# Optimization experiments

Measured on AMD Instinct MI355X. Metric: run time of the kernel, lower is better.

## Reference

```python
import jax, jax.numpy as jnp
import numpy as np

T, N, F0, H0, H1 = 8, 50000, 128, 128, 64
NNZ, E = 800000, 1000000


def setup_inputs() -> dict:
    key = jax.random.key(0)
    ks = jax.random.split(key, 24)
    s = 0.05  # param scale so sigmoid/tanh gates are not fully saturated
    inp = {
        "X": jax.random.normal(ks[0], (T, N, F0), jnp.float32),
        "A_rows": jax.random.randint(ks[1], (T, NNZ), 0, N, jnp.int32),
        "A_cols": jax.random.randint(ks[2], (T, NNZ), 0, N, jnp.int32),
        "A_val": jax.random.uniform(ks[3], (T, NNZ), jnp.float32),
        "edge_time": jax.random.randint(ks[4], (E,), 0, T, jnp.int32),
        "edge_src": jax.random.randint(ks[5], (E,), 0, N, jnp.int32),
        "edge_trg": jax.random.randint(ks[6], (E,), 0, N, jnp.int32),
        "p": jax.random.normal(ks[7], (F0,), jnp.float32),
        "W_Z": s * jax.random.normal(ks[8], (F0, F0), jnp.float32),
        "U_Z": s * jax.random.normal(ks[9], (F0, F0), jnp.float32),
        "B_Z": s * jax.random.normal(ks[10], (F0, H0), jnp.float32),
        "W_R": s * jax.random.normal(ks[11], (F0, F0), jnp.float32),
        "U_R": s * jax.random.normal(ks[12], (F0, F0), jnp.float32),
        "B_R": s * jax.random.normal(ks[13], (F0, H0), jnp.float32),
        "W_H": s * jax.random.normal(ks[14], (F0, F0), jnp.float32),
        "U_H": s * jax.random.normal(ks[15], (F0, F0), jnp.float32),
        "B_H": s * jax.random.normal(ks[16], (F0, H0), jnp.float32),
        "W_init": s * jax.random.normal(ks[17], (F0, H0), jnp.float32),
        "U": s * jax.random.normal(ks[18], (2 * H0, H1), jnp.float32),
    }
    return inp


def reference(X, A_rows, A_cols, A_val, edge_time, edge_src, edge_trg,
              p, W_Z, U_Z, B_Z, W_R, U_R, B_R, W_H, U_H, B_H, W_init, U):
    Tn, Nn, _ = X.shape
    k = W_init.shape[1]  # topk size == columns of evolving weight
    p_hat = p / jnp.linalg.norm(p)

    def step(W, inputs):
        Xs, rows, cols, vals = inputs  # Xs: [N,F0]; rows/cols/vals: [NNZ]
        # summarize: top-k node rows weighted by projection score
        y = Xs @ p_hat                       # [N]
        topv, idx = jax.lax.top_k(y, k)
        Z = (Xs[idx] * topv[:, None]).T      # [F0,k]
        # GRU-style weight evolution on the [F0,k] weight matrix
        Zg = jax.nn.sigmoid(W_Z @ Z + U_Z @ W + B_Z)
        R = jax.nn.sigmoid(W_R @ Z + U_R @ W + B_R)
        Ht = jnp.tanh(W_H @ Z + U_H @ (R * W) + B_H)
        W_new = (1.0 - Zg) * W + Zg * Ht
        # sparse GCN conv: (A @ Xs) @ W_new  via gather + segment_sum
        AH = jax.ops.segment_sum(vals[:, None] * Xs[cols], rows,
                                 num_segments=Nn)  # [N,F0]
        return W_new, AH @ W_new                   # Y_t: [N,H0]

    W_fin, Y = jax.lax.scan(step, W_init, (X, A_rows, A_cols, A_val))
    Yf = Y.reshape(Tn * Nn, -1)                    # [T*N,H0]
    flat_src = edge_time * Nn + edge_src
    flat_trg = edge_time * Nn + edge_trg
    Y_mat = jnp.concatenate([Yf[flat_src], Yf[flat_trg]], axis=1)  # [E,2*H0]
    output = Y_mat @ U                              # [E,H1]
    return output, W_fin
```

## Files before the change

### kernel.cpp

```cpp
#include <hip/hip_runtime.h>
#include <math.h>

#define T_ 8
#define N_ 50000
#define F0_ 128
#define H0_ 128
#define H1_ 64
#define NNZ_ 800000
#define E_ 1000000
#define K_ 128
#define CAP_ 3072
#define NB 391
#define BCH 8192

__device__ inline unsigned ford(float f) {
    unsigned b = __float_as_uint(f);
    return (b & 0x80000000u) ? ~b : (b | 0x80000000u);
}
__device__ inline float funord(unsigned u) {
    unsigned b = (u & 0x80000000u) ? (u & 0x7fffffffu) : ~u;
    return __uint_as_float(b);
}
__device__ inline unsigned bfr(float f) {
    unsigned u = __float_as_uint(f);
    return (u + 0x7fffu + ((u >> 16) & 1u)) >> 16;
}
__device__ inline unsigned bfpack(float lo, float hi) { return bfr(lo) | (bfr(hi) << 16); }
__device__ inline float bflo(unsigned u) { return __uint_as_float(u << 16); }
__device__ inline float bfhi(unsigned u) { return __uint_as_float(u & 0xffff0000u); }

__global__ void k_phat(const float* p, float* p_hat) {
    __shared__ float s[128];
    int i = threadIdx.x;
    float v = p[i];
    s[i] = v * v;
    __syncthreads();
    for (int off = 64; off > 0; off >>= 1) {
        if (i < off) s[i] += s[i + off];
        __syncthreads();
    }
    p_hat[i] = v / sqrtf(s[0]);
}

__global__ void k_y(const float* __restrict__ X, const float* __restrict__ p_hat,
                    float* __restrict__ y, unsigned* __restrict__ Xh) {
    int gid = blockIdx.x * 256 + threadIdx.x;
    int wave = gid >> 6, lane = gid & 63;
    if (wave >= T_ * N_) return;
    const float2* xr = (const float2*)(X + (size_t)wave * F0_);
    float2 a = xr[lane];
    if (Xh) Xh[(size_t)wave * 64 + lane] = bfpack(a.x, a.y);
    float2 ph = ((const float2*)p_hat)[lane];
    float acc = a.x * ph.x + a.y * ph.y;
#pragma unroll
    for (int off = 32; off > 0; off >>= 1) acc += __shfl_down(acc, off);
    if (lane == 0) y[wave] = acc;
}

__global__ __launch_bounds__(1024) void k_topk(const float* __restrict__ y,
                                               float* __restrict__ topv,
                                               int* __restrict__ topidx) {
    int t = blockIdx.x;
    const float* yt = y + (size_t)t * N_;
    __shared__ int hist[256];
    __shared__ int sb1, sAbove, sP, scand;
    __shared__ unsigned cu[CAP_];
    __shared__ int cidx[CAP_];
    int tid = threadIdx.x;

    if (tid < 256) hist[tid] = 0;
    __syncthreads();
    for (int i = tid; i < N_; i += 1024) {
        unsigned u = ford(yt[i]);
        atomicAdd(&hist[u >> 24], 1);
    }
    __syncthreads();
    if (tid == 0) {
        int acc = 0, b = 255;
        for (; b >= 0; b--) { acc += hist[b]; if (acc >= K_) break; }
        sb1 = b;
        sAbove = acc - hist[b];
    }
    __syncthreads();
    int b1 = sb1;
    if (tid < 256) hist[tid] = 0;
    __syncthreads();
    for (int i = tid; i < N_; i += 1024) {
        unsigned u = ford(yt[i]);
        if ((int)(u >> 24) == b1) atomicAdd(&hist[(u >> 16) & 255], 1);
    }
    __syncthreads();
    if (tid == 0) {
        int acc = sAbove, b = 255;
        for (; b >= 0; b--) { acc += hist[b]; if (acc >= K_) break; }
        sP = (b1 << 8) | b;
        scand = 0;
    }
    __syncthreads();
    unsigned P = (unsigned)sP;
    for (int i = tid; i < N_; i += 1024) {
        unsigned u = ford(yt[i]);
        if ((u >> 16) >= P) {
            int pos = atomicAdd(&scand, 1);
            if (pos < CAP_) { cu[pos] = u; cidx[pos] = i; }
        }
    }
    __syncthreads();
    int C = min(scand, CAP_);
    for (int c = tid; c < C; c += 1024) {
        unsigned uc = cu[c];
        int ic = cidx[c];
        int rank = 0;
        for (int o = 0; o < C; o++) {
            unsigned uo = cu[o];
            rank += (uo > uc) || (uo == uc && cidx[o] < ic);
        }
        if (rank < K_) {
            topv[t * K_ + rank] = funord(uc);
            topidx[t * K_ + rank] = ic;
        }
    }
}

__global__ void k_z(const float* __restrict__ X, const float* __restrict__ topv,
                    const int* __restrict__ topidx, float* __restrict__ Z) {
    int gid = blockIdx.x * 256 + threadIdx.x;
    if (gid >= T_ * F0_ * K_) return;
    int j = gid & 127;
    int f = (gid >> 7) & 127;
    int t = gid >> 14;
    int idx = topidx[t * K_ + j];
    float v = topv[t * K_ + j];
    Z[gid] = X[((size_t)(t * N_ + idx)) * F0_ + f] * v;
}

__global__ void k_az(const float* __restrict__ WZ, const float* __restrict__ WR,
                     const float* __restrict__ WH, const float* __restrict__ BZ,
                     const float* __restrict__ BR, const float* __restrict__ BH,
                     const float* __restrict__ Z, float* __restrict__ AZ,
                     float* __restrict__ AR, float* __restrict__ AHo) {
    int gid = blockIdx.x * 256 + threadIdx.x;
    int j = gid & 127;
    int i = (gid >> 7) & 127;
    int t = (gid >> 14) & 7;
    int g = gid >> 17;
    const float* W = (g == 0) ? WZ : (g == 1) ? WR : WH;
    const float* B = (g == 0) ? BZ : (g == 1) ? BR : BH;
    float* Ao = (g == 0) ? AZ : (g == 1) ? AR : AHo;
    const float* Zt = Z + (size_t)t * 16384;
    float acc = B[i * 128 + j];
    for (int k = 0; k < 128; k++) acc += W[i * 128 + k] * Zt[k * 128 + j];
    Ao[(size_t)(t * 128 + i) * 128 + j] = acc;
}

__global__ __launch_bounds__(512) void k_cnt(const int* __restrict__ A_rows,
                                             int* __restrict__ bcnt) {
    __shared__ int cnt[NB];
    int t = blockIdx.y, ci = blockIdx.x;
    int tid = threadIdx.x;
    for (int i = tid; i < NB; i += 512) cnt[i] = 0;
    __syncthreads();
    int e0 = ci * BCH;
#pragma unroll
    for (int k = 0; k < 16; k++) {
        int idx = e0 + tid + k * 512;
        if (idx < NNZ_) atomicAdd(&cnt[A_rows[(size_t)t * NNZ_ + idx] >> 7], 1);
    }
    __syncthreads();
    for (int b = tid; b < NB; b += 512)
        if (cnt[b]) atomicAdd(&bcnt[t * NB + b], cnt[b]);
}

__global__ __launch_bounds__(512) void k_bscan(const int* __restrict__ bcnt,
                                               int* __restrict__ bbase) {
    int t = blockIdx.x;
    int tid = threadIdx.x;
    __shared__ int buf[512];
    int v = (tid < NB) ? bcnt[t * NB + tid] : 0;
    buf[tid] = v;
    __syncthreads();
    for (int off = 1; off < 512; off <<= 1) {
        int x = (tid >= off) ? buf[tid - off] : 0;
        __syncthreads();
        buf[tid] += x;
        __syncthreads();
    }
    if (tid < NB) bbase[t * NB + tid] = buf[tid] - v;
}

__global__ __launch_bounds__(512) void k_binA(const int* __restrict__ A_rows,
                                              const int* __restrict__ A_cols,
                                              const float* __restrict__ A_val,
                                              const int* __restrict__ bbase,
                                              int* __restrict__ bfill,
                                              int2* __restrict__ ebuck) {
    __shared__ int cnt[NB];
    __shared__ int gbase[NB];
    __shared__ int rbase[NB];
    int t = blockIdx.y, ci = blockIdx.x;
    int tid = threadIdx.x;
    for (int i = tid; i < NB; i += 512) cnt[i] = 0;
    __syncthreads();
    unsigned meta[16];
    float val[16];
    int lrank[16];
    int e0 = ci * BCH;
#pragma unroll
    for (int k = 0; k < 16; k++) {
        int idx = e0 + tid + k * 512;
        meta[k] = 0xFFFFFFFFu;
        val[k] = 0.f;
        lrank[k] = 0;
        if (idx < NNZ_) {
            int r = A_rows[(size_t)t * NNZ_ + idx];
            int c = A_cols[(size_t)t * NNZ_ + idx];
            val[k] = A_val[(size_t)t * NNZ_ + idx];
            int b = r >> 7, rlo = r & 127;
            meta[k] = (unsigned)c | ((unsigned)rlo << 16) | ((unsigned)b << 23);
            lrank[k] = atomicAdd(&cnt[b], 1);
        }
    }
    __syncthreads();
    for (int b = tid; b < NB; b += 512) {
        int n = cnt[b];
        gbase[b] = n ? atomicAdd(&bfill[t * NB + b], n) : 0;
        rbase[b] = bbase[t * NB + b];
    }
    __syncthreads();
#pragma unroll
    for (int k = 0; k < 16; k++) {
        if (meta[k] != 0xFFFFFFFFu) {
            int b = meta[k] >> 23;
            ebuck[(size_t)t * NNZ_ + rbase[b] + gbase[b] + lrank[k]] =
                make_int2((int)meta[k], __float_as_int(val[k]));
        }
    }
}

__global__ __launch_bounds__(256) void k_bsort(const int* __restrict__ bbase,
                                               const int* __restrict__ bcnt,
                                               const int2* __restrict__ ebuck,
                                               int2* __restrict__ ecv,
                                               int* __restrict__ row_ptr) {
    __shared__ int rcnt[128];
    __shared__ int rex[128];
    __shared__ int rfill[128];
    __shared__ int sbuf[128];
    int t = blockIdx.y, b = blockIdx.x;
    int tid = threadIdx.x;
    int r0 = b << 7;
    int nrows = min(128, N_ - r0);
    int base = bbase[t * NB + b];
    int n = bcnt[t * NB + b];
    if (tid < 128) {
        rcnt[tid] = 0;
        rfill[tid] = 0;
    }
    __syncthreads();
    const int2* src = ebuck + (size_t)t * NNZ_ + base;
    int2* dst = ecv + (size_t)t * NNZ_ + base;
    for (int i = tid; i < n; i += 256) atomicAdd(&rcnt[(src[i].x >> 16) & 127], 1);
    __syncthreads();
    if (tid < 128) sbuf[tid] = rcnt[tid];
    __syncthreads();
    for (int off = 1; off < 128; off <<= 1) {
        int x = (tid >= off && tid < 128) ? sbuf[tid - off] : 0;
        __syncthreads();
        if (tid < 128) sbuf[tid] += x;
        __syncthreads();
    }
    if (tid < 128) rex[tid] = sbuf[tid] - rcnt[tid];
    if (tid < nrows) row_ptr[(size_t)t * (N_ + 1) + r0 + tid] = base + sbuf[tid] - rcnt[tid];
    if (b == 0 && tid == 0) row_ptr[(size_t)t * (N_ + 1) + N_] = NNZ_;
    __syncthreads();
    for (int i = tid; i < n; i += 256) {
        int2 e = src[i];
        int rlo = (e.x >> 16) & 127;
        int col = e.x & 0xFFFF;
        int pos = rex[rlo] + atomicAdd(&rfill[rlo], 1);
        dst[pos] = make_int2(col, e.y);
    }
}

__global__ void k_spmm(const unsigned* __restrict__ Xh, const int* __restrict__ row_ptr,
                       const int2* __restrict__ ecv, float* __restrict__ AH) {
    int gid = blockIdx.x * 256 + threadIdx.x;
    int wave = gid >> 6, lane = gid & 63;
    if (wave >= T_ * N_) return;
    int t = wave / N_;
    int r = wave - t * N_;
    int s = row_ptr[(size_t)t * (N_ + 1) + r];
    int len = row_ptr[(size_t)t * (N_ + 1) + r + 1] - s;
    const unsigned* Xt = Xh + (size_t)t * N_ * 64 + lane;
    const int2* ev = ecv + (size_t)t * NNZ_;
    float2 acc = {0.f, 0.f};
    for (int base = 0; base < len; base += 64) {
        int nn = min(64, len - base);
        int2 my = {0, 0};
        if (base + lane < len) my = ev[s + base + lane];
        int q = 0;
        for (; q + 8 <= nn; q += 8) {
            int c0 = __shfl(my.x, q + 0); float v0 = __int_as_float(__shfl(my.y, q + 0));
            int c1 = __shfl(my.x, q + 1); float v1 = __int_as_float(__shfl(my.y, q + 1));
            int c2 = __shfl(my.x, q + 2); float v2 = __int_as_float(__shfl(my.y, q + 2));
            int c3 = __shfl(my.x, q + 3); float v3 = __int_as_float(__shfl(my.y, q + 3));
            int c4 = __shfl(my.x, q + 4); float v4 = __int_as_float(__shfl(my.y, q + 4));
            int c5 = __shfl(my.x, q + 5); float v5 = __int_as_float(__shfl(my.y, q + 5));
            int c6 = __shfl(my.x, q + 6); float v6 = __int_as_float(__shfl(my.y, q + 6));
            int c7 = __shfl(my.x, q + 7); float v7 = __int_as_float(__shfl(my.y, q + 7));
            unsigned x0 = Xt[(size_t)c0 * 64];
            unsigned x1 = Xt[(size_t)c1 * 64];
            unsigned x2 = Xt[(size_t)c2 * 64];
            unsigned x3 = Xt[(size_t)c3 * 64];
            unsigned x4 = Xt[(size_t)c4 * 64];
            unsigned x5 = Xt[(size_t)c5 * 64];
            unsigned x6 = Xt[(size_t)c6 * 64];
            unsigned x7 = Xt[(size_t)c7 * 64];
            acc.x += v0 * bflo(x0); acc.y += v0 * bfhi(x0);
            acc.x += v1 * bflo(x1); acc.y += v1 * bfhi(x1);
            acc.x += v2 * bflo(x2); acc.y += v2 * bfhi(x2);
            acc.x += v3 * bflo(x3); acc.y += v3 * bfhi(x3);
            acc.x += v4 * bflo(x4); acc.y += v4 * bfhi(x4);
            acc.x += v5 * bflo(x5); acc.y += v5 * bfhi(x5);
            acc.x += v6 * bflo(x6); acc.y += v6 * bfhi(x6);
            acc.x += v7 * bflo(x7); acc.y += v7 * bfhi(x7);
        }
        for (; q < nn; q++) {
            int c = __shfl(my.x, q);
            float v = __int_as_float(__shfl(my.y, q));
            unsigned xp = Xt[(size_t)c * 64];
            acc.x += v * bflo(xp);
            acc.y += v * bfhi(xp);
        }
    }
    ((float2*)AH)[(size_t)wave * 64 + lane] = acc;
}

__global__ void k_spmm_f32(const float* __restrict__ X, const int* __restrict__ row_ptr,
                           const int2* __restrict__ ecv, float* __restrict__ AH) {
    int gid = blockIdx.x * 256 + threadIdx.x;
    int wave = gid >> 6, lane = gid & 63;
    if (wave >= T_ * N_) return;
    int t = wave / N_;
    int r = wave - t * N_;
    int s = row_ptr[(size_t)t * (N_ + 1) + r];
    int len = row_ptr[(size_t)t * (N_ + 1) + r + 1] - s;
    const float2* Xt = (const float2*)(X + (size_t)t * N_ * F0_);
    const int2* ev = ecv + (size_t)t * NNZ_;
    float2 acc = {0.f, 0.f};
    for (int base = 0; base < len; base += 64) {
        int nn = min(64, len - base);
        int2 my = {0, 0};
        if (base + lane < len) my = ev[s + base + lane];
        for (int q = 0; q < nn; q++) {
            int c = __shfl(my.x, q);
            float v = __int_as_float(__shfl(my.y, q));
            float2 x = Xt[(size_t)c * 64 + lane];
            acc.x += v * x.x;
            acc.y += v * x.y;
        }
    }
    ((float2*)AH)[(size_t)wave * 64 + lane] = acc;
}

__global__ __launch_bounds__(256) void k_gru(const float* __restrict__ AZt,
                                             const float* __restrict__ ARt,
                                             const float* __restrict__ AHt,
                                             const float* __restrict__ UZ,
                                             const float* __restrict__ UR,
                                             const float* __restrict__ UH,
                                             const float* __restrict__ Wprev,
                                             float* __restrict__ Wnew) {
    __shared__ float RWs[128][2];
    int jl = threadIdx.x >> 7;
    int i = threadIdx.x & 127;
    int j = blockIdx.x * 2 + jl;
    int gid = i * 128 + j;
    float az = AZt[gid], ar = ARt[gid];
    for (int k = 0; k < 128; k++) {
        float w = Wprev[k * 128 + j];
        az += UZ[i * 128 + k] * w;
        ar += UR[i * 128 + k] * w;
    }
    float zg = 1.f / (1.f + expf(-az));
    float rg = 1.f / (1.f + expf(-ar));
    RWs[i][jl] = rg * Wprev[gid];
    __syncthreads();
    float acc = AHt[gid];
    for (int k = 0; k < 128; k++) acc += UH[i * 128 + k] * RWs[k][jl];
    float ht = tanhf(acc);
    float w0 = Wprev[gid];
    Wnew[gid] = (1.f - zg) * w0 + zg * ht;
}

__global__ void k_wu(const float* __restrict__ W_seq, const float* __restrict__ U,
                     float* __restrict__ WU) {
    int blk = blockIdx.x;
    int t = blk >> 7, k = blk & 127;
    int h2 = threadIdx.x;
    const float* Wt = W_seq + (size_t)t * 16384;
    int h = h2 & 63;
    const float* Ub = U + (h2 < 64 ? 0 : 128 * 64);
    float acc = 0.f;
    for (int m = 0; m < 128; m++) acc += Wt[k * 128 + m] * Ub[m * 64 + h];
    WU[((size_t)t * 128 + k) * 128 + h2] = acc;
}

__global__ __launch_bounds__(256) void k_pq(const float* __restrict__ AH,
                                            const float* __restrict__ WU,
                                            unsigned* __restrict__ PQh) {
    __shared__ float AT[32][36];
    __shared__ float WUc[32][128];
    int t = blockIdx.y;
    int rbase = blockIdx.x * 32;
    int tid = threadIdx.x;
    const float* wu = WU + (size_t)t * 16384;
    const float* AHt = AH + (size_t)t * N_ * F0_;
    unsigned* PQt = PQh + (size_t)t * N_ * 64;
    int cg = tid & 31;
    int rg = tid >> 5;
    float4 acc0 = {0.f, 0.f, 0.f, 0.f};
    float4 acc1 = {0.f, 0.f, 0.f, 0.f};
    float4 acc2 = {0.f, 0.f, 0.f, 0.f};
    float4 acc3 = {0.f, 0.f, 0.f, 0.f};
    int srow = tid >> 3;
    int sk4 = (tid & 7) * 4;
    for (int kc = 0; kc < 128; kc += 32) {
        {
            float4 v = {0.f, 0.f, 0.f, 0.f};
            int r = rbase + srow;
            if (r < N_) v = *(const float4*)(AHt + (size_t)r * F0_ + kc + sk4);
            AT[sk4 + 0][srow] = v.x;
            AT[sk4 + 1][srow] = v.y;
            AT[sk4 + 2][srow] = v.z;
            AT[sk4 + 3][srow] = v.w;
        }
        {
            const float4* src = (const float4*)(wu + (size_t)kc * 128);
            float4* dst = (float4*)&WUc[0][0];
            dst[tid] = src[tid];
            dst[tid + 256] = src[tid + 256];
            dst[tid + 512] = src[tid + 512];
            dst[tid + 768] = src[tid + 768];
        }
        __syncthreads();
#pragma unroll 4
        for (int kk = 0; kk < 32; kk++) {
            float4 a = *(const float4*)&AT[kk][rg * 4];
            float4 w = *(const float4*)&WUc[kk][cg * 4];
            acc0.x += a.x * w.x; acc0.y += a.x * w.y; acc0.z += a.x * w.z; acc0.w += a.x * w.w;
            acc1.x += a.y * w.x; acc1.y += a.y * w.y; acc1.z += a.y * w.z; acc1.w += a.y * w.w;
            acc2.x += a.z * w.x; acc2.y += a.z * w.y; acc2.z += a.z * w.z; acc2.w += a.z * w.w;
            acc3.x += a.w * w.x; acc3.y += a.w * w.y; acc3.z += a.w * w.z; acc3.w += a.w * w.w;
        }
        __syncthreads();
    }
    int r0 = rbase + rg * 4;
    if (r0 + 0 < N_) {
        uint2 o = {bfpack(acc0.x, acc0.y), bfpack(acc0.z, acc0.w)};
        *(uint2*)(PQt + (size_t)(r0 + 0) * 64 + cg * 2) = o;
    }
    if (r0 + 1 < N_) {
        uint2 o = {bfpack(acc1.x, acc1.y), bfpack(acc1.z, acc1.w)};
        *(uint2*)(PQt + (size_t)(r0 + 1) * 64 + cg * 2) = o;
    }
    if (r0 + 2 < N_) {
        uint2 o = {bfpack(acc2.x, acc2.y), bfpack(acc2.z, acc2.w)};
        *(uint2*)(PQt + (size_t)(r0 + 2) * 64 + cg * 2) = o;
    }
    if (r0 + 3 < N_) {
        uint2 o = {bfpack(acc3.x, acc3.y), bfpack(acc3.z, acc3.w)};
        *(uint2*)(PQt + (size_t)(r0 + 3) * 64 + cg * 2) = o;
    }
}

__global__ __launch_bounds__(256) void k_pq_f32(float* __restrict__ AH,
                                                const float* __restrict__ WU) {
    __shared__ float AT[32][36];
    __shared__ float WUc[32][128];
    int t = blockIdx.y;
    int rbase = blockIdx.x * 32;
    int tid = threadIdx.x;
    const float* wu = WU + (size_t)t * 16384;
    float* AHt = AH + (size_t)t * N_ * F0_;
    int cg = tid & 31;
    int rg = tid >> 5;
    float4 acc0 = {0.f, 0.f, 0.f, 0.f};
    float4 acc1 = {0.f, 0.f, 0.f, 0.f};
    float4 acc2 = {0.f, 0.f, 0.f, 0.f};
    float4 acc3 = {0.f, 0.f, 0.f, 0.f};
    int srow = tid >> 3;
    int sk4 = (tid & 7) * 4;
    for (int kc = 0; kc < 128; kc += 32) {
        {
            float4 v = {0.f, 0.f, 0.f, 0.f};
            int r = rbase + srow;
            if (r < N_) v = *(const float4*)(AHt + (size_t)r * F0_ + kc + sk4);
            AT[sk4 + 0][srow] = v.x;
            AT[sk4 + 1][srow] = v.y;
            AT[sk4 + 2][srow] = v.z;
            AT[sk4 + 3][srow] = v.w;
        }
        {
            const float4* src = (const float4*)(wu + (size_t)kc * 128);
            float4* dst = (float4*)&WUc[0][0];
            dst[tid] = src[tid];
            dst[tid + 256] = src[tid + 256];
            dst[tid + 512] = src[tid + 512];
            dst[tid + 768] = src[tid + 768];
        }
        __syncthreads();
#pragma unroll 4
        for (int kk = 0; kk < 32; kk++) {
            float4 a = *(const float4*)&AT[kk][rg * 4];
            float4 w = *(const float4*)&WUc[kk][cg * 4];
            acc0.x += a.x * w.x; acc0.y += a.x * w.y; acc0.z += a.x * w.z; acc0.w += a.x * w.w;
            acc1.x += a.y * w.x; acc1.y += a.y * w.y; acc1.z += a.y * w.z; acc1.w += a.y * w.w;
            acc2.x += a.z * w.x; acc2.y += a.z * w.y; acc2.z += a.z * w.z; acc2.w += a.z * w.w;
            acc3.x += a.w * w.x; acc3.y += a.w * w.y; acc3.z += a.w * w.z; acc3.w += a.w * w.w;
        }
        __syncthreads();
    }
    int r0 = rbase + rg * 4;
    if (r0 + 0 < N_) *(float4*)(AHt + (size_t)(r0 + 0) * F0_ + cg * 4) = acc0;
    if (r0 + 1 < N_) *(float4*)(AHt + (size_t)(r0 + 1) * F0_ + cg * 4) = acc1;
    if (r0 + 2 < N_) *(float4*)(AHt + (size_t)(r0 + 2) * F0_ + cg * 4) = acc2;
    if (r0 + 3 < N_) *(float4*)(AHt + (size_t)(r0 + 3) * F0_ + cg * 4) = acc3;
}

__global__ void k_final(const unsigned* __restrict__ PQh, const int* __restrict__ et,
                        const int* __restrict__ es, const int* __restrict__ eg,
                        float* __restrict__ out) {
    int gid = blockIdx.x * 256 + threadIdx.x;
    if (gid >= E_ * 16) return;
    int e = gid >> 4, q = gid & 15;
    int t = et[e];
    const uint2 a = *(const uint2*)(PQh + ((size_t)(t * N_ + es[e])) * 64 + q * 2);
    const uint2 b = *(const uint2*)(PQh + ((size_t)(t * N_ + eg[e])) * 64 + 32 + q * 2);
    float4 o;
    o.x = bflo(a.x) + bflo(b.x);
    o.y = bfhi(a.x) + bfhi(b.x);
    o.z = bflo(a.y) + bflo(b.y);
    o.w = bfhi(a.y) + bfhi(b.y);
    *(float4*)(out + (size_t)e * 64 + q * 4) = o;
}

__global__ void k_final_f32(const float* __restrict__ PQ, const int* __restrict__ et,
                            const int* __restrict__ es, const int* __restrict__ eg,
                            float* __restrict__ out) {
    int gid = blockIdx.x * 256 + threadIdx.x;
    if (gid >= E_ * 16) return;
    int e = gid >> 4, q = gid & 15;
    int t = et[e];
    const float4 a = *(const float4*)(PQ + ((size_t)(t * N_ + es[e])) * 128 + q * 4);
    const float4 b = *(const float4*)(PQ + ((size_t)(t * N_ + eg[e])) * 128 + 64 + q * 4);
    float4 o = {a.x + b.x, a.y + b.y, a.z + b.z, a.w + b.w};
    *(float4*)(out + (size_t)e * 64 + q * 4) = o;
}

__global__ void k_wfin(const float* __restrict__ W_seq, float* __restrict__ out) {
    int gid = blockIdx.x * 256 + threadIdx.x;
    out[(size_t)E_ * 64 + gid] = W_seq[(size_t)7 * 16384 + gid];
}

extern "C" void kernel_launch(void* const* d_in, const int* in_sizes, int n_in,
                              void* d_out, int out_size, void* d_ws, size_t ws_size,
                              hipStream_t stream) {
    const float* X = (const float*)d_in[0];
    const int* A_rows = (const int*)d_in[1];
    const int* A_cols = (const int*)d_in[2];
    const float* A_val = (const float*)d_in[3];
    const int* edge_time = (const int*)d_in[4];
    const int* edge_src = (const int*)d_in[5];
    const int* edge_trg = (const int*)d_in[6];
    const float* p = (const float*)d_in[7];
    const float* W_Z = (const float*)d_in[8];
    const float* U_Z = (const float*)d_in[9];
    const float* B_Z = (const float*)d_in[10];
    const float* W_R = (const float*)d_in[11];
    const float* U_R = (const float*)d_in[12];
    const float* B_R = (const float*)d_in[13];
    const float* W_H = (const float*)d_in[14];
    const float* U_H = (const float*)d_in[15];
    const float* B_H = (const float*)d_in[16];
    const float* W_init = (const float*)d_in[17];
    const float* U = (const float*)d_in[18];
    float* out = (float*)d_out;

    char* ws = (char*)d_ws;
    size_t off = 0;
    auto take = [&](size_t bytes) {
        char* ptr = ws + off;
        off = (off + bytes + 255) & ~(size_t)255;
        return (void*)ptr;
    };
    float* AH = (float*)take((size_t)T_ * N_ * F0_ * 4);
    int2* ecv = (int2*)take((size_t)T_ * NNZ_ * 8);
    float* yv = (float*)take((size_t)T_ * N_ * 4);
    int* row_ptr = (int*)take((size_t)T_ * (N_ + 1) * 4);
    int* bcnt = (int*)take((size_t)T_ * NB * 4);
    int* bbase = (int*)take((size_t)T_ * NB * 4);
    int* bfill = (int*)take((size_t)T_ * NB * 4);
    float* p_hat = (float*)take(512);
    float* topv = (float*)take((size_t)T_ * K_ * 4);
    int* topidx = (int*)take((size_t)T_ * K_ * 4);
    float* Z = (float*)take((size_t)T_ * F0_ * K_ * 4);
    float* AZb = (float*)take((size_t)T_ * 16384 * 4);
    float* ARb = (float*)take((size_t)T_ * 16384 * 4);
    float* AHb = (float*)take((size_t)T_ * 16384 * 4);
    float* W_seq = (float*)take((size_t)T_ * 16384 * 4);
    float* WU = (float*)take((size_t)T_ * 16384 * 4);
    unsigned* Xh = (unsigned*)take((size_t)T_ * N_ * 64 * 4);
    bool use_bf16 = (off <= ws_size);
    unsigned* PQh = Xh;
    int2* ebuck = (int2*)AH;

    hipMemsetAsync(bcnt, 0, (size_t)T_ * NB * 4, stream);
    hipMemsetAsync(bfill, 0, (size_t)T_ * NB * 4, stream);

    k_phat<<<1, 128, 0, stream>>>(p, p_hat);
    k_y<<<(T_ * N_ * 64) / 256, 256, 0, stream>>>(X, p_hat, yv, use_bf16 ? Xh : nullptr);
    k_topk<<<T_, 1024, 0, stream>>>(yv, topv, topidx);
    k_z<<<(T_ * F0_ * K_) / 256, 256, 0, stream>>>(X, topv, topidx, Z);
    k_az<<<(3 * T_ * 16384) / 256, 256, 0, stream>>>(W_Z, W_R, W_H, B_Z, B_R, B_H, Z,
                                                     AZb, ARb, AHb);
    {
        dim3 gA((NNZ_ + BCH - 1) / BCH, T_);
        k_cnt<<<gA, 512, 0, stream>>>(A_rows, bcnt);
        k_bscan<<<T_, 512, 0, stream>>>(bcnt, bbase);
        k_binA<<<gA, 512, 0, stream>>>(A_rows, A_cols, A_val, bbase, bfill, ebuck);
        dim3 gB(NB, T_);
        k_bsort<<<gB, 256, 0, stream>>>(bbase, bcnt, ebuck, ecv, row_ptr);
    }
    if (use_bf16)
        k_spmm<<<(T_ * N_ * 64) / 256, 256, 0, stream>>>(Xh, row_ptr, ecv, AH);
    else
        k_spmm_f32<<<(T_ * N_ * 64) / 256, 256, 0, stream>>>(X, row_ptr, ecv, AH);
    for (int t = 0; t < T_; t++) {
        const float* Wprev = (t == 0) ? W_init : (W_seq + (size_t)(t - 1) * 16384);
        k_gru<<<64, 256, 0, stream>>>(AZb + (size_t)t * 16384, ARb + (size_t)t * 16384,
                                      AHb + (size_t)t * 16384, U_Z, U_R, U_H, Wprev,
                                      W_seq + (size_t)t * 16384);
    }
    k_wu<<<T_ * 128, 128, 0, stream>>>(W_seq, U, WU);
    {
        dim3 g((N_ + 31) / 32, T_);
        if (use_bf16) {
            k_pq<<<g, 256, 0, stream>>>(AH, WU, PQh);
            k_final<<<(E_ * 16) / 256, 256, 0, stream>>>(PQh, edge_time, edge_src,
                                                         edge_trg, out);
        } else {
            k_pq_f32<<<g, 256, 0, stream>>>(AH, WU);
            k_final_f32<<<(E_ * 16) / 256, 256, 0, stream>>>(AH, edge_time, edge_src,
                                                             edge_trg, out);
        }
    }
    k_wfin<<<(F0_ * H0_) / 256, 256, 0, stream>>>(W_seq, out);
}
```

Baseline: 966.5 us.

## Reassociate GCN as A·(X·WU) so SpMM gathers bf16 projected features

Rather than computing AH = A·X in fp32 and then multiplying by WU, the code first computes X·WU densely from the bf16 X copy and stores it as bf16, then runs the sparse gather-accumulate over those rows and writes PQ in bf16. The aim is to halve the SpMM output write (bf16 instead of fp32 AH) and to drop the fp32 AH read in the dense GEMM, since that GEMM now reads bf16 X. It also adds a 16-wide unrolled gather loop. The intermediate X·WU is rounded to bf16 before aggregation, which adds rounding error, and the workspace layout is reorganised so XWU and PQh share the old AH region.

```diff
diff --git a/kernel.cpp b/kernel.cpp
--- a/kernel.cpp
+++ b/kernel.cpp
@@ -282,8 +282,76 @@
     }
 }
 
-__global__ void k_spmm(const unsigned* __restrict__ Xh, const int* __restrict__ row_ptr,
-                       const int2* __restrict__ ecv, float* __restrict__ AH) {
+__global__ __launch_bounds__(256) void k_xwu(const unsigned* __restrict__ Xh,
+                                             const float* __restrict__ WU,
+                                             unsigned* __restrict__ XWU) {
+    __shared__ float AT[32][36];
+    __shared__ float WUc[32][128];
+    int t = blockIdx.y;
+    int rbase = blockIdx.x * 32;
+    int tid = threadIdx.x;
+    const float* wu = WU + (size_t)t * 16384;
+    const unsigned* Xt = Xh + (size_t)t * N_ * 64;
+    unsigned* XWUt = XWU + (size_t)t * N_ * 64;
+    int cg = tid & 31;
+    int rg = tid >> 5;
+    float4 acc0 = {0.f, 0.f, 0.f, 0.f};
+    float4 acc1 = {0.f, 0.f, 0.f, 0.f};
+    float4 acc2 = {0.f, 0.f, 0.f, 0.f};
+    float4 acc3 = {0.f, 0.f, 0.f, 0.f};
+    int srow = tid >> 3;
+    int sk4 = (tid & 7) * 4;
+    for (int kc = 0; kc < 128; kc += 32) {
+        {
+            uint2 u = {0u, 0u};
+            int r = rbase + srow;
+            if (r < N_) u = *(const uint2*)(Xt + (size_t)r * 64 + (kc >> 1) + (sk4 >> 1));
+            AT[sk4 + 0][srow] = bflo(u.x);
+            AT[sk4 + 1][srow] = bfhi(u.x);
+            AT[sk4 + 2][srow] = bflo(u.y);
+            AT[sk4 + 3][srow] = bfhi(u.y);
+        }
+        {
+            const float4* src = (const float4*)(wu + (size_t)kc * 128);
+            float4* dst = (float4*)&WUc[0][0];
+            dst[tid] = src[tid];
+            dst[tid + 256] = src[tid + 256];
+            dst[tid + 512] = src[tid + 512];
+            dst[tid + 768] = src[tid + 768];
+        }
+        __syncthreads();
+#pragma unroll 4
+        for (int kk = 0; kk < 32; kk++) {
+            float4 a = *(const float4*)&AT[kk][rg * 4];
+            float4 w = *(const float4*)&WUc[kk][cg * 4];
+            acc0.x += a.x * w.x; acc0.y += a.x * w.y; acc0.z += a.x * w.z; acc0.w += a.x * w.w;
+            acc1.x += a.y * w.x; acc1.y += a.y * w.y; acc1.z += a.y * w.z; acc1.w += a.y * w.w;
+            acc2.x += a.z * w.x; acc2.y += a.z * w.y; acc2.z += a.z * w.z; acc2.w += a.z * w.w;
+            acc3.x += a.w * w.x; acc3.y += a.w * w.y; acc3.z += a.w * w.z; acc3.w += a.w * w.w;
+        }
+        __syncthreads();
+    }
+    int r0 = rbase + rg * 4;
+    if (r0 + 0 < N_) {
+        uint2 o = {bfpack(acc0.x, acc0.y), bfpack(acc0.z, acc0.w)};
+        *(uint2*)(XWUt + (size_t)(r0 + 0) * 64 + cg * 2) = o;
+    }
+    if (r0 + 1 < N_) {
+        uint2 o = {bfpack(acc1.x, acc1.y), bfpack(acc1.z, acc1.w)};
+        *(uint2*)(XWUt + (size_t)(r0 + 1) * 64 + cg * 2) = o;
+    }
+    if (r0 + 2 < N_) {
+        uint2 o = {bfpack(acc2.x, acc2.y), bfpack(acc2.z, acc2.w)};
+        *(uint2*)(XWUt + (size_t)(r0 + 2) * 64 + cg * 2) = o;
+    }
+    if (r0 + 3 < N_) {
+        uint2 o = {bfpack(acc3.x, acc3.y), bfpack(acc3.z, acc3.w)};
+        *(uint2*)(XWUt + (size_t)(r0 + 3) * 64 + cg * 2) = o;
+    }
+}
+
+__global__ void k_spmm2(const unsigned* __restrict__ XWU, const int* __restrict__ row_ptr,
+                        const int2* __restrict__ ecv, unsigned* __restrict__ PQh) {
     int gid = blockIdx.x * 256 + threadIdx.x;
     int wave = gid >> 6, lane = gid & 63;
     if (wave >= T_ * N_) return;
@@ -291,7 +359,7 @@
     int r = wave - t * N_;
     int s = row_ptr[(size_t)t * (N_ + 1) + r];
     int len = row_ptr[(size_t)t * (N_ + 1) + r + 1] - s;
-    const unsigned* Xt = Xh + (size_t)t * N_ * 64 + lane;
+    const unsigned* Xt = XWU + (size_t)t * N_ * 64 + lane;
     const int2* ev = ecv + (size_t)t * NNZ_;
     float2 acc = {0.f, 0.f};
     for (int base = 0; base < len; base += 64) {
@@ -299,6 +367,56 @@
         int2 my = {0, 0};
         if (base + lane < len) my = ev[s + base + lane];
         int q = 0;
+        for (; q + 16 <= nn; q += 16) {
+            int c0 = __shfl(my.x, q + 0);  float v0 = __int_as_float(__shfl(my.y, q + 0));
+            int c1 = __shfl(my.x, q + 1);  float v1 = __int_as_float(__shfl(my.y, q + 1));
+            int c2 = __shfl(my.x, q + 2);  float v2 = __int_as_float(__shfl(my.y, q + 2));
+            int c3 = __shfl(my.x, q + 3);  float v3 = __int_as_float(__shfl(my.y, q + 3));
+            int c4 = __shfl(my.x, q + 4);  float v4 = __int_as_float(__shfl(my.y, q + 4));
+            int c5 = __shfl(my.x, q + 5);  float v5 = __int_as_float(__shfl(my.y, q + 5));
+            int c6 = __shfl(my.x, q + 6);  float v6 = __int_as_float(__shfl(my.y, q + 6));
+            int c7 = __shfl(my.x, q + 7);  float v7 = __int_as_float(__shfl(my.y, q + 7));
+            int c8 = __shfl(my.x, q + 8);  float v8 = __int_as_float(__shfl(my.y, q + 8));
+            int c9 = __shfl(my.x, q + 9);  float v9 = __int_as_float(__shfl(my.y, q + 9));
+            int cA = __shfl(my.x, q + 10); float vA = __int_as_float(__shfl(my.y, q + 10));
+            int cB = __shfl(my.x, q + 11); float vB = __int_as_float(__shfl(my.y, q + 11));
+            int cC = __shfl(my.x, q + 12); float vC = __int_as_float(__shfl(my.y, q + 12));
+            int cD = __shfl(my.x, q + 13); float vD = __int_as_float(__shfl(my.y, q + 13));
+            int cE = __shfl(my.x, q + 14); float vE = __int_as_float(__shfl(my.y, q + 14));
+            int cF = __shfl(my.x, q + 15); float vF = __int_as_float(__shfl(my.y, q + 15));
+            unsigned x0 = Xt[(size_t)c0 * 64];
+            unsigned x1 = Xt[(size_t)c1 * 64];
+            unsigned x2 = Xt[(size_t)c2 * 64];
+            unsigned x3 = Xt[(size_t)c3 * 64];
+            unsigned x4 = Xt[(size_t)c4 * 64];
+            unsigned x5 = Xt[(size_t)c5 * 64];
+            unsigned x6 = Xt[(size_t)c6 * 64];
+            unsigned x7 = Xt[(size_t)c7 * 64];
+            unsigned x8 = Xt[(size_t)c8 * 64];
+            unsigned x9 = Xt[(size_t)c9 * 64];
+            unsigned xA = Xt[(size_t)cA * 64];
+            unsigned xB = Xt[(size_t)cB * 64];
+            unsigned xC = Xt[(size_t)cC * 64];
+            unsigned xD = Xt[(size_t)cD * 64];
+            unsigned xE = Xt[(size_t)cE * 64];
+            unsigned xF = Xt[(size_t)cF * 64];
+            acc.x += v0 * bflo(x0); acc.y += v0 * bfhi(x0);
+            acc.x += v1 * bflo(x1); acc.y += v1 * bfhi(x1);
+            acc.x += v2 * bflo(x2); acc.y += v2 * bfhi(x2);
+            acc.x += v3 * bflo(x3); acc.y += v3 * bfhi(x3);
+            acc.x += v4 * bflo(x4); acc.y += v4 * bfhi(x4);
+            acc.x += v5 * bflo(x5); acc.y += v5 * bfhi(x5);
+            acc.x += v6 * bflo(x6); acc.y += v6 * bfhi(x6);
+            acc.x += v7 * bflo(x7); acc.y += v7 * bfhi(x7);
+            acc.x += v8 * bflo(x8); acc.y += v8 * bfhi(x8);
+            acc.x += v9 * bflo(x9); acc.y += v9 * bfhi(x9);
+            acc.x += vA * bflo(xA); acc.y += vA * bfhi(xA);
+            acc.x += vB * bflo(xB); acc.y += vB * bfhi(xB);
+            acc.x += vC * bflo(xC); acc.y += vC * bfhi(xC);
+            acc.x += vD * bflo(xD); acc.y += vD * bfhi(xD);
+            acc.x += vE * bflo(xE); acc.y += vE * bfhi(xE);
+            acc.x += vF * bflo(xF); acc.y += vF * bfhi(xF);
+        }
         for (; q + 8 <= nn; q += 8) {
             int c0 = __shfl(my.x, q + 0); float v0 = __int_as_float(__shfl(my.y, q + 0));
             int c1 = __shfl(my.x, q + 1); float v1 = __int_as_float(__shfl(my.y, q + 1));
@@ -333,7 +451,7 @@
             acc.y += v * bfhi(xp);
         }
     }
-    ((float2*)AH)[(size_t)wave * 64 + lane] = acc;
+    PQh[(size_t)wave * 64 + lane] = bfpack(acc.x, acc.y);
 }
 
 __global__ void k_spmm_f32(const float* __restrict__ X, const int* __restrict__ row_ptr,
@@ -404,74 +522,6 @@
     float acc = 0.f;
     for (int m = 0; m < 128; m++) acc += Wt[k * 128 + m] * Ub[m * 64 + h];
     WU[((size_t)t * 128 + k) * 128 + h2] = acc;
-}
-
-__global__ __launch_bounds__(256) void k_pq(const float* __restrict__ AH,
-                                            const float* __restrict__ WU,
-                                            unsigned* __restrict__ PQh) {
-    __shared__ float AT[32][36];
-    __shared__ float WUc[32][128];
-    int t = blockIdx.y;
-    int rbase = blockIdx.x * 32;
-    int tid = threadIdx.x;
-    const float* wu = WU + (size_t)t * 16384;
-    const float* AHt = AH + (size_t)t * N_ * F0_;
-    unsigned* PQt = PQh + (size_t)t * N_ * 64;
-    int cg = tid & 31;
-    int rg = tid >> 5;
-    float4 acc0 = {0.f, 0.f, 0.f, 0.f};
-    float4 acc1 = {0.f, 0.f, 0.f, 0.f};
-    float4 acc2 = {0.f, 0.f, 0.f, 0.f};
-    float4 acc3 = {0.f, 0.f, 0.f, 0.f};
-    int srow = tid >> 3;
-    int sk4 = (tid & 7) * 4;
-    for (int kc = 0; kc < 128; kc += 32) {
-        {
-            float4 v = {0.f, 0.f, 0.f, 0.f};
-            int r = rbase + srow;
-            if (r < N_) v = *(const float4*)(AHt + (size_t)r * F0_ + kc + sk4);
-            AT[sk4 + 0][srow] = v.x;
-            AT[sk4 + 1][srow] = v.y;
-            AT[sk4 + 2][srow] = v.z;
-            AT[sk4 + 3][srow] = v.w;
-        }
-        {
-            const float4* src = (const float4*)(wu + (size_t)kc * 128);
-            float4* dst = (float4*)&WUc[0][0];
-            dst[tid] = src[tid];
-            dst[tid + 256] = src[tid + 256];
-            dst[tid + 512] = src[tid + 512];
-            dst[tid + 768] = src[tid + 768];
-        }
-        __syncthreads();
-#pragma unroll 4
-        for (int kk = 0; kk < 32; kk++) {
-            float4 a = *(const float4*)&AT[kk][rg * 4];
-            float4 w = *(const float4*)&WUc[kk][cg * 4];
-            acc0.x += a.x * w.x; acc0.y += a.x * w.y; acc0.z += a.x * w.z; acc0.w += a.x * w.w;
-            acc1.x += a.y * w.x; acc1.y += a.y * w.y; acc1.z += a.y * w.z; acc1.w += a.y * w.w;
-            acc2.x += a.z * w.x; acc2.y += a.z * w.y; acc2.z += a.z * w.z; acc2.w += a.z * w.w;
-            acc3.x += a.w * w.x; acc3.y += a.w * w.y; acc3.z += a.w * w.z; acc3.w += a.w * w.w;
-        }
-        __syncthreads();
-    }
-    int r0 = rbase + rg * 4;
-    if (r0 + 0 < N_) {
-        uint2 o = {bfpack(acc0.x, acc0.y), bfpack(acc0.z, acc0.w)};
-        *(uint2*)(PQt + (size_t)(r0 + 0) * 64 + cg * 2) = o;
-    }
-    if (r0 + 1 < N_) {
-        uint2 o = {bfpack(acc1.x, acc1.y), bfpack(acc1.z, acc1.w)};
-        *(uint2*)(PQt + (size_t)(r0 + 1) * 64 + cg * 2) = o;
-    }
-    if (r0 + 2 < N_) {
-        uint2 o = {bfpack(acc2.x, acc2.y), bfpack(acc2.z, acc2.w)};
-        *(uint2*)(PQt + (size_t)(r0 + 2) * 64 + cg * 2) = o;
-    }
-    if (r0 + 3 < N_) {
-        uint2 o = {bfpack(acc3.x, acc3.y), bfpack(acc3.z, acc3.w)};
-        *(uint2*)(PQt + (size_t)(r0 + 3) * 64 + cg * 2) = o;
-    }
 }
 
 __global__ __launch_bounds__(256) void k_pq_f32(float* __restrict__ AH,
@@ -594,7 +644,7 @@
         off = (off + bytes + 255) & ~(size_t)255;
         return (void*)ptr;
     };
-    float* AH = (float*)take((size_t)T_ * N_ * F0_ * 4);
+    float* AHreg = (float*)take((size_t)T_ * N_ * F0_ * 4);
     int2* ecv = (int2*)take((size_t)T_ * NNZ_ * 8);
     float* yv = (float*)take((size_t)T_ * N_ * 4);
     int* row_ptr = (int*)take((size_t)T_ * (N_ + 1) * 4);
@@ -612,8 +662,9 @@
     float* WU = (float*)take((size_t)T_ * 16384 * 4);
     unsigned* Xh = (unsigned*)take((size_t)T_ * N_ * 64 * 4);
     bool use_bf16 = (off <= ws_size);
-    unsigned* PQh = Xh;
-    int2* ebuck = (int2*)AH;
+    int2* ebuck = (int2*)AHreg;
+    unsigned* XWU = (unsigned*)AHreg;
+    unsigned* PQh = XWU + (size_t)T_ * N_ * 64;
 
     hipMemsetAsync(bcnt, 0, (size_t)T_ * NB * 4, stream);
     hipMemsetAsync(bfill, 0, (size_t)T_ * NB * 4, stream);
@@ -632,10 +683,6 @@
         dim3 gB(NB, T_);
         k_bsort<<<gB, 256, 0, stream>>>(bbase, bcnt, ebuck, ecv, row_ptr);
     }
-    if (use_bf16)
-        k_spmm<<<(T_ * N_ * 64) / 256, 256, 0, stream>>>(Xh, row_ptr, ecv, AH);
-    else
-        k_spmm_f32<<<(T_ * N_ * 64) / 256, 256, 0, stream>>>(X, row_ptr, ecv, AH);
     for (int t = 0; t < T_; t++) {
         const float* Wprev = (t == 0) ? W_init : (W_seq + (size_t)(t - 1) * 16384);
         k_gru<<<64, 256, 0, stream>>>(AZb + (size_t)t * 16384, ARb + (size_t)t * 16384,
@@ -643,17 +690,19 @@
                                       W_seq + (size_t)t * 16384);
     }
     k_wu<<<T_ * 128, 128, 0, stream>>>(W_seq, U, WU);
-    {
+    if (use_bf16) {
         dim3 g((N_ + 31) / 32, T_);
-        if (use_bf16) {
-            k_pq<<<g, 256, 0, stream>>>(AH, WU, PQh);
-            k_final<<<(E_ * 16) / 256, 256, 0, stream>>>(PQh, edge_time, edge_src,
+        k_xwu<<<g, 256, 0, stream>>>(Xh, WU, XWU);
+        k_spmm2<<<(T_ * N_ * 64) / 256, 256, 0, stream>>>(XWU, row_ptr, ecv, PQh);
+        k_final<<<(E_ * 16) / 256, 256, 0, stream>>>(PQh, edge_time, edge_src,
+                                                     edge_trg, out);
+    } else {
+        float* AH = AHreg;
+        k_spmm_f32<<<(T_ * N_ * 64) / 256, 256, 0, stream>>>(X, row_ptr, ecv, AH);
+        dim3 g((N_ + 31) / 32, T_);
+        k_pq_f32<<<g, 256, 0, stream>>>(AH, WU);
+        k_final_f32<<<(E_ * 16) / 256, 256, 0, stream>>>(AH, edge_time, edge_src,
                                                          edge_trg, out);
-        } else {
-            k_pq_f32<<<g, 256, 0, stream>>>(AH, WU);
-            k_final_f32<<<(E_ * 16) / 256, 256, 0, stream>>>(AH, edge_time, edge_src,
-                                                             edge_trg, out);
-        }
     }
     k_wfin<<<(F0_ * H0_) / 256, 256, 0, stream>>>(W_seq, out);
 }
```

Measured after the change: 954.4 us. About the same (-1.3%).
